# Performance work log

Measured on AMD Instinct MI355X. Metric: run time of the kernel, lower is better.

The kernel has to match this reference:

```python
import jax, jax.numpy as jnp
import numpy as np

B, N, F, U, S = 64, 4096, 2, 16, 2


def setup_inputs() -> dict:
    key = jax.random.key(0)
    ks = jax.random.split(key, 7)
    inputs = jax.random.normal(ks[0], (B, F * N), dtype=jnp.float32)
    state = jax.random.normal(ks[1], (B, U * N), dtype=jnp.float32)

    def random_walk(k):
        a = jax.random.uniform(k, (N, N), dtype=jnp.float32)
        return a / jnp.sum(a, axis=1, keepdims=True)  # row-stochastic like D^-1 A

    support0 = random_walk(ks[2])
    support1 = random_walk(ks[3])
    kshape = ((F + U) * S, U)
    scale = jnp.float32(1.0 / np.sqrt(kshape[0]))
    r_kernel = jax.random.normal(ks[4], kshape, dtype=jnp.float32) * scale
    u_kernel = jax.random.normal(ks[5], kshape, dtype=jnp.float32) * scale
    c_kernel = jax.random.normal(ks[6], kshape, dtype=jnp.float32) * scale
    return {"inputs": inputs, "state": state, "support0": support0,
            "support1": support1, "r_kernel": r_kernel, "u_kernel": u_kernel,
            "c_kernel": c_kernel}


def _diffuse(x, supports):
    # x: (B, C, N); K.dot(x, support.T)[b,c,m] = sum_n x[b,c,n] * support[m,n]
    return jnp.concatenate([jnp.einsum('bcn,mn->bcm', x, s) for s in supports], axis=1)


def reference(inputs, state, support0, support1, r_kernel, u_kernel, c_kernel):
    supports = (support0, support1)
    feats = inputs.reshape(B, F, N)
    prev = state.reshape(B, U, N)

    h = _diffuse(feats, supports).transpose(0, 2, 1)   # (B, N, S*F)
    st = _diffuse(prev, supports).transpose(0, 2, 1)   # (B, N, S*U)
    hs = jnp.concatenate([h, st], axis=-1)             # (B, N, S*(F+U))

    r = jax.nn.sigmoid(hs @ r_kernel)                  # (B, N, U)
    u = jax.nn.sigmoid(hs @ u_kernel)                  # (B, N, U)

    prev_t = prev.transpose(0, 2, 1)                   # (B, N, U)
    r_prev = (r * prev_t).transpose(0, 2, 1)           # (B, U, N)
    c_state = _diffuse(r_prev, supports).transpose(0, 2, 1)  # (B, N, S*U)
    c = jnp.tanh(jnp.concatenate([h, c_state], axis=-1) @ c_kernel)  # (B, N, U)

    z = u * prev_t + (1.0 - u) * c                     # (B, N, U)
    # original: activation=None -> linear, then K.reshape(output, (-1, units*num_nodes))
    return z.reshape(B, U * N)
```

## Files before the change

### kernel.cpp

```cpp
#include <hip/hip_runtime.h>
#include <cstdint>

#define KDIM 4096
#define NNODE 4096
#define TSTEPS 128

typedef __bf16 bf16x8 __attribute__((ext_vector_type(8)));
typedef float floatx4 __attribute__((ext_vector_type(4)));

__device__ __forceinline__ uint16_t f2b(float f) {
  union { float f; uint32_t u; } v; v.f = f;
  uint32_t u = v.u;
  return (uint16_t)((u + 0x7FFFu + ((u >> 16) & 1u)) >> 16);
}
__device__ __forceinline__ float b2f(uint16_t h) {
  union { uint32_t u; float f; } v; v.u = ((uint32_t)h) << 16; return v.f;
}
__device__ __forceinline__ uint32_t pack2(float a, float b) {
  return (uint32_t)f2b(a) | ((uint32_t)f2b(b) << 16);
}


__global__ __launch_bounds__(256) void cvt_supports(
    const float* __restrict__ s0, const float* __restrict__ s1,
    uint16_t* __restrict__ d0, uint16_t* __restrict__ d1) {
  const float* src = blockIdx.z ? s1 : s0;
  uint16_t* dst = blockIdx.z ? d1 : d0;
  const int c16 = blockIdx.x;
  const int t = blockIdx.y * 4 + (threadIdx.x >> 6);
  const int lane = threadIdx.x & 63;
  const int mr = lane & 15, q = lane >> 4;
  const float* p = src + (size_t)(c16 * 16 + mr) * KDIM + t * 32 + q * 8;
  float4 v0 = *(const float4*)p;
  float4 v1 = *(const float4*)(p + 4);
  uint4 o;
  o.x = pack2(v0.x, v0.y); o.y = pack2(v0.z, v0.w);
  o.z = pack2(v1.x, v1.y); o.w = pack2(v1.z, v1.w);
  *(uint4*)(dst + ((size_t)(c16 * 128 + t)) * 512 + (size_t)lane * 8) = o;
}

__global__ __launch_bounds__(256) void pack_x1(
    const float* __restrict__ inp, const float* __restrict__ st,
    uint16_t* __restrict__ X1) {
  const int r16 = blockIdx.x;
  const int t = blockIdx.y * 4 + (threadIdx.x >> 6);
  const int lane = threadIdx.x & 63;
  const int mr = lane & 15, q = lane >> 4;
  const int row = r16 * 16 + mr;
  int b = row / 18, c = row - b * 18;
  const float* p = (c < 2) ? (inp + (size_t)b * 8192 + (size_t)c * 4096)
                           : (st + (size_t)b * 65536 + (size_t)(c - 2) * 4096);
  p += t * 32 + q * 8;
  float4 v0 = *(const float4*)p;
  float4 v1 = *(const float4*)(p + 4);
  uint4 o;
  o.x = pack2(v0.x, v0.y); o.y = pack2(v0.z, v0.w);
  o.z = pack2(v1.x, v1.y); o.w = pack2(v1.z, v1.w);
  *(uint4*)(X1 + ((size_t)(r16 * 128 + t)) * 512 + (size_t)lane * 8) = o;
}

__device__ __forceinline__ void gl_lds16(const uint16_t* g, uint16_t* l) {
  __builtin_amdgcn_global_load_lds(
      (const __attribute__((address_space(1))) uint32_t*)g,
      (__attribute__((address_space(3))) uint32_t*)l, 16, 0, 0);
}

template <int MODE>
__global__ __launch_bounds__(512, 2) void gemm_frag(
    const uint16_t* __restrict__ Af, const uint16_t* __restrict__ S0f,
    const uint16_t* __restrict__ S1f, uint16_t* __restrict__ D) {
  constexpr int CPB   = (MODE == 1) ? 18 : 16;
  constexpr int OUTC  = (MODE == 1) ? 36 : 32;
  constexpr int MFR   = (MODE == 1) ? 9 : 8;
  constexpr int WM    = (MODE == 1) ? 1 : 2;
  constexpr int WN    = 8 / WM;
  constexpr int AR    = MFR / WM;
  constexpr int BR    = 16 / WN;
  constexpr int NREAL = MFR + 16;
  constexpr int SLOTS = (NREAL + 7) & ~7;
  constexpr int LPW   = SLOTS / 8;
  constexpr int NCH   = TSTEPS;

  __shared__ uint16_t sAB[4][SLOTS][512];

  const int lane = threadIdx.x & 63, wave = threadIdx.x >> 6;
  const int wr = wave / WN, wc = wave % WN;
  const int s = blockIdx.z;
  const uint16_t* __restrict__ Bf = s ? S1f : S0f;
  const int yF = blockIdx.y * MFR;
  const int xF = blockIdx.x * 16;

  const uint16_t* Gp[LPW];
#pragma unroll
  for (int i = 0; i < LPW; ++i) {
    int sid = wave * LPW + i;
    const uint16_t* base;
    int fr;
    if (sid < MFR)        { base = Af; fr = yF + sid; }
    else if (sid < NREAL) { base = Bf; fr = xF + sid - MFR; }
    else                  { base = Af; fr = yF; }
    Gp[i] = base + (size_t)fr * (TSTEPS * 512) + (size_t)lane * 8;
  }

  floatx4 acc[AR][BR];
#pragma unroll
  for (int i = 0; i < AR; ++i)
#pragma unroll
    for (int j = 0; j < BR; ++j) acc[i][j] = (floatx4){0.f, 0.f, 0.f, 0.f};

  auto STAGE = [&](int bi, int c) {
    uint16_t* l = &sAB[bi][wave * LPW][0];
    const size_t off = (size_t)c * 512;
#pragma unroll
    for (int i = 0; i < LPW; ++i)
      gl_lds16(Gp[i] + off, l + (size_t)i * 512);
  };

  auto LDREG = [&](int bi, bf16x8* a, bf16x8* b) {
    const uint16_t* base = &sAB[bi][0][lane * 8];
#pragma unroll
    for (int rt = 0; rt < AR; ++rt)
      a[rt] = *(const bf16x8*)(base + (size_t)(wr * AR + rt) * 512);
#pragma unroll
    for (int ct = 0; ct < BR; ++ct)
      b[ct] = *(const bf16x8*)(base + (size_t)(MFR + wc * BR + ct) * 512);
  };

  auto MFMAALL = [&](bf16x8* a, bf16x8* b) {
    __builtin_amdgcn_s_setprio(1);
#pragma unroll
    for (int rt = 0; rt < AR; ++rt)
#pragma unroll
      for (int ct = 0; ct < BR; ++ct)
        acc[rt][ct] = __builtin_amdgcn_mfma_f32_16x16x32_bf16(
            a[rt], b[ct], acc[rt][ct], 0, 0, 0);
    __builtin_amdgcn_s_setprio(0);
  };

  auto waitVM = [&] {
    if constexpr (MODE == 1) asm volatile("s_waitcnt vmcnt(8)" ::: "memory");
    else                     asm volatile("s_waitcnt vmcnt(6)" ::: "memory");
  };
  auto waitLG = [&] {
    if constexpr (MODE == 1) asm volatile("s_waitcnt lgkmcnt(11)" ::: "memory");
    else                     asm volatile("s_waitcnt lgkmcnt(8)" ::: "memory");
  };

  STAGE(0, 0);
  STAGE(1, 1);
  STAGE(2, 2);
  waitVM();
  __builtin_amdgcn_sched_barrier(0);
  __builtin_amdgcn_s_barrier();
  __builtin_amdgcn_sched_barrier(0);
  bf16x8 aA[AR], bA[BR], aB[AR], bB[BR];
  LDREG(0, aA, bA);

#define GITER(J, SB, RB, CA, CB, NA, NB)                                    \
  {                                                                         \
    int cl = c0 + 3 + (J);                                                  \
    if (cl > NCH - 1) cl = NCH - 1;       \
    STAGE((SB), cl);                                                        \
    waitVM();                                                               \
    __builtin_amdgcn_sched_barrier(0);                                      \
    __builtin_amdgcn_s_barrier();                                           \
    __builtin_amdgcn_sched_barrier(0);                                      \
    LDREG((RB), NA, NB);                                                    \
    waitLG();                                                               \
    __builtin_amdgcn_sched_barrier(0);                                      \
    MFMAALL(CA, CB);                                                        \
    __builtin_amdgcn_sched_barrier(0);                                      \
  }

  for (int m = 0; m < NCH / 4; ++m) {
    const int c0 = m * 4;
    GITER(0, 3, 1, aA, bA, aB, bB)
    GITER(1, 0, 2, aB, bB, aA, bA)
    GITER(2, 1, 3, aA, bA, aB, bB)
    GITER(3, 2, 0, aB, bB, aA, bA)
  }
#undef GITER

#pragma unroll
  for (int rt = 0; rt < AR; ++rt) {
#pragma unroll
    for (int r = 0; r < 4; ++r) {
      int rowg = (yF + wr * AR + rt) * 16 + (lane >> 4) * 4 + r;
      int b = rowg / CPB, c = rowg - b * CPB;
      int jj;
      if (MODE == 1) jj = (c < 2) ? (2 * s + c) : (4 + 16 * s + (c - 2));
      else jj = 16 * s + c;
      uint16_t* drow = D + (size_t)(b * OUTC + jj) * NNODE;
#pragma unroll
      for (int ct = 0; ct < BR; ++ct) {
        int colg = xF * 16 + (wc * BR + ct) * 16 + (lane & 15);
        drow[colg] = f2b(acc[rt][ct][r]);
      }
    }
  }
}

__global__ __launch_bounds__(256) void stage2(
    const uint16_t* __restrict__ P1, const float* __restrict__ state,
    const float* __restrict__ rk, const float* __restrict__ uk,
    uint16_t* __restrict__ X2f, float* __restrict__ U) {
  __shared__ float s_rk[576], s_uk[576];
  __shared__ uint16_t s_x2[16 * 264];
  for (int i = threadIdx.x; i < 576; i += 256) { s_rk[i] = rk[i]; s_uk[i] = uk[i]; }
  __syncthreads();
  const int b = blockIdx.x >> 4, nb = blockIdx.x & 15;
  const int i = threadIdx.x;
  const int n = nb * 256 + i;
  float hs[36];
  const uint16_t* p = P1 + (size_t)b * 36 * NNODE + n;
#pragma unroll
  for (int j = 0; j < 36; ++j)
    hs[j] = b2f(p[(size_t)j * NNODE]);
  float ar[16], au[16];
#pragma unroll
  for (int k = 0; k < 16; ++k) { ar[k] = 0.f; au[k] = 0.f; }
#pragma unroll
  for (int j = 0; j < 36; ++j) {
    float h = hs[j];
#pragma unroll
    for (int k = 0; k < 16; ++k) {
      ar[k] += h * s_rk[j * 16 + k];
      au[k] += h * s_uk[j * 16 + k];
    }
  }
  const float* sp = state + (size_t)b * 65536 + n;
#pragma unroll
  for (int k = 0; k < 16; ++k) {
    float r = 1.f / (1.f + __expf(-ar[k]));
    float uu = 1.f / (1.f + __expf(-au[k]));
    float prev = sp[(size_t)k * NNODE];
    s_x2[k * 264 + i] = f2b(r * prev);
    U[(size_t)(b * 16 + k) * NNODE + n] = uu;
  }
  __syncthreads();
  uint16_t* region = X2f + ((size_t)b * 128 + nb * 8) * 512;
#pragma unroll
  for (int rr = 0; rr < 2; ++rr) {
    int fid = rr * 256 + i;
    int kk = fid & 15, qq = (fid >> 4) & 3, tl = fid >> 6;
    uint4 v = *(const uint4*)&s_x2[kk * 264 + tl * 32 + qq * 8];
    *(uint4*)(region + (size_t)fid * 8) = v;
  }
}

__global__ __launch_bounds__(256) void stage4(
    const uint16_t* __restrict__ P1, const uint16_t* __restrict__ P3,
    const float* __restrict__ U, const float* __restrict__ state,
    const float* __restrict__ ck, float* __restrict__ out) {
  __shared__ float s_ck[576];
  for (int i = threadIdx.x; i < 576; i += 256) s_ck[i] = ck[i];
  __syncthreads();
  int idx = blockIdx.x * 256 + threadIdx.x;
  int b = idx >> 12, n = idx & 4095;
  float hv[36];
  const uint16_t* p1 = P1 + (size_t)b * 36 * NNODE + n;
#pragma unroll
  for (int j = 0; j < 4; ++j)
    hv[j] = b2f(p1[(size_t)j * NNODE]);
  const uint16_t* p3 = P3 + (size_t)b * 32 * NNODE + n;
#pragma unroll
  for (int j = 0; j < 32; ++j)
    hv[4 + j] = b2f(p3[(size_t)j * NNODE]);
  float ac[16];
#pragma unroll
  for (int k = 0; k < 16; ++k) ac[k] = 0.f;
#pragma unroll
  for (int j = 0; j < 36; ++j) {
    float h = hv[j];
#pragma unroll
    for (int k = 0; k < 16; ++k) ac[k] += h * s_ck[j * 16 + k];
  }
  const float* sp = state + (size_t)b * 65536 + n;
  const float* up = U + (size_t)b * 16 * NNODE + n;
  float z[16];
#pragma unroll
  for (int k = 0; k < 16; ++k) {
    float e = __expf(2.f * ac[k]);
    float c = 1.f - 2.f / (e + 1.f);
    float uu = up[(size_t)k * NNODE];
    float prev = sp[(size_t)k * NNODE];
    z[k] = uu * prev + (1.f - uu) * c;
  }
  float4* po = (float4*)(out + (size_t)b * 65536 + (size_t)n * 16);
#pragma unroll
  for (int k4 = 0; k4 < 4; ++k4)
    po[k4] = make_float4(z[k4 * 4], z[k4 * 4 + 1], z[k4 * 4 + 2], z[k4 * 4 + 3]);
}

extern "C" void kernel_launch(void* const* d_in, const int* in_sizes, int n_in,
                              void* d_out, int out_size, void* d_ws, size_t ws_size,
                              hipStream_t stream) {
  const float* inputs = (const float*)d_in[0];
  const float* state = (const float*)d_in[1];
  const float* s0 = (const float*)d_in[2];
  const float* s1 = (const float*)d_in[3];
  const float* rk = (const float*)d_in[4];
  const float* uk = (const float*)d_in[5];
  const float* ck = (const float*)d_in[6];
  float* out = (float*)d_out;
  char* ws = (char*)d_ws;

  uint16_t* S0f = (uint16_t*)(ws);
  uint16_t* S1f = (uint16_t*)(ws + 33554432);
  uint16_t* X1f = (uint16_t*)(ws + 67108864);
  uint16_t* X2f = (uint16_t*)(ws + 67108864);
  uint16_t* P1 = (uint16_t*)(ws + 76546048);
  float* U = (float*)(ws + 114294784);
  uint16_t* P3 = (uint16_t*)(ws + 131072000);

  cvt_supports<<<dim3(256, 32, 2), 256, 0, stream>>>(s0, s1, S0f, S1f);
  pack_x1<<<dim3(72, 32), 256, 0, stream>>>(inputs, state, X1f);
  gemm_frag<1><<<dim3(16, 8, 2), 512, 0, stream>>>(X1f, S0f, S1f, P1);
  stage2<<<1024, 256, 0, stream>>>(P1, state, rk, uk, X2f, U);
  gemm_frag<3><<<dim3(16, 8, 2), 512, 0, stream>>>(X2f, S0f, S1f, P3);
  stage4<<<1024, 256, 0, stream>>>(P1, P3, U, state, ck, out);
}
```

Baseline: 352.5 us.

## Split-K the second diffusion GEMM with larger M tiles and merge pack kernels

The second GEMM now doubles its per-block M fragment count (8 to 16) and splits the K dimension in two. Each half writes bf16 partials to separate buffers, and stage4 sums them. This gives more B reuse per block while keeping the grid at 256 blocks. The two fp32-to-bf16 pack kernels are also fused into one launch to cut launch overhead. In exchange, the extra partial buffer adds memory traffic, and rounding each partial to bf16 separately adds some precision loss.

```diff
diff --git a/kernel.cpp b/kernel.cpp
--- a/kernel.cpp
+++ b/kernel.cpp
@@ -21,42 +21,38 @@
 }
 
 
-__global__ __launch_bounds__(256) void cvt_supports(
+__global__ __launch_bounds__(256) void pack_all(
+    const float* __restrict__ inp, const float* __restrict__ st,
     const float* __restrict__ s0, const float* __restrict__ s1,
-    uint16_t* __restrict__ d0, uint16_t* __restrict__ d1) {
-  const float* src = blockIdx.z ? s1 : s0;
-  uint16_t* dst = blockIdx.z ? d1 : d0;
-  const int c16 = blockIdx.x;
+    uint16_t* __restrict__ X1, uint16_t* __restrict__ d0,
+    uint16_t* __restrict__ d1) {
   const int t = blockIdx.y * 4 + (threadIdx.x >> 6);
   const int lane = threadIdx.x & 63;
   const int mr = lane & 15, q = lane >> 4;
-  const float* p = src + (size_t)(c16 * 16 + mr) * KDIM + t * 32 + q * 8;
+  const float* p;
+  uint16_t* dst;
+  if (blockIdx.z < 2) {
+    const float* src = blockIdx.z ? s1 : s0;
+    uint16_t* d = blockIdx.z ? d1 : d0;
+    const int c16 = blockIdx.x;
+    p = src + (size_t)(c16 * 16 + mr) * KDIM + t * 32 + q * 8;
+    dst = d + ((size_t)(c16 * 128 + t)) * 512 + (size_t)lane * 8;
+  } else {
+    const int r16 = blockIdx.x;
+    if (r16 >= 72) return;
+    const int row = r16 * 16 + mr;
+    int b = row / 18, c = row - b * 18;
+    const float* pb = (c < 2) ? (inp + (size_t)b * 8192 + (size_t)c * 4096)
+                              : (st + (size_t)b * 65536 + (size_t)(c - 2) * 4096);
+    p = pb + t * 32 + q * 8;
+    dst = X1 + ((size_t)(r16 * 128 + t)) * 512 + (size_t)lane * 8;
+  }
   float4 v0 = *(const float4*)p;
   float4 v1 = *(const float4*)(p + 4);
   uint4 o;
   o.x = pack2(v0.x, v0.y); o.y = pack2(v0.z, v0.w);
   o.z = pack2(v1.x, v1.y); o.w = pack2(v1.z, v1.w);
-  *(uint4*)(dst + ((size_t)(c16 * 128 + t)) * 512 + (size_t)lane * 8) = o;
-}
-
-__global__ __launch_bounds__(256) void pack_x1(
-    const float* __restrict__ inp, const float* __restrict__ st,
-    uint16_t* __restrict__ X1) {
-  const int r16 = blockIdx.x;
-  const int t = blockIdx.y * 4 + (threadIdx.x >> 6);
-  const int lane = threadIdx.x & 63;
-  const int mr = lane & 15, q = lane >> 4;
-  const int row = r16 * 16 + mr;
-  int b = row / 18, c = row - b * 18;
-  const float* p = (c < 2) ? (inp + (size_t)b * 8192 + (size_t)c * 4096)
-                           : (st + (size_t)b * 65536 + (size_t)(c - 2) * 4096);
-  p += t * 32 + q * 8;
-  float4 v0 = *(const float4*)p;
-  float4 v1 = *(const float4*)(p + 4);
-  uint4 o;
-  o.x = pack2(v0.x, v0.y); o.y = pack2(v0.z, v0.w);
-  o.z = pack2(v1.x, v1.y); o.w = pack2(v1.z, v1.w);
-  *(uint4*)(X1 + ((size_t)(r16 * 128 + t)) * 512 + (size_t)lane * 8) = o;
+  *(uint4*)dst = o;
 }
 
 __device__ __forceinline__ void gl_lds16(const uint16_t* g, uint16_t* l) {
@@ -71,21 +67,26 @@
     const uint16_t* __restrict__ S1f, uint16_t* __restrict__ D) {
   constexpr int CPB   = (MODE == 1) ? 18 : 16;
   constexpr int OUTC  = (MODE == 1) ? 36 : 32;
-  constexpr int MFR   = (MODE == 1) ? 9 : 8;
+  constexpr int MFR   = (MODE == 1) ? 9 : 16;
   constexpr int WM    = (MODE == 1) ? 1 : 2;
   constexpr int WN    = 8 / WM;
   constexpr int AR    = MFR / WM;
   constexpr int BR    = 16 / WN;
   constexpr int NREAL = MFR + 16;
-  constexpr int SLOTS = (NREAL + 7) & ~7;
+  constexpr int SLOTS = 32;
   constexpr int LPW   = SLOTS / 8;
-  constexpr int NCH   = TSTEPS;
+  constexpr int KSP   = (MODE == 1) ? 1 : 2;
+  constexpr int NCH   = TSTEPS / KSP;
+  constexpr size_t PSTRIDE = (size_t)64 * OUTC * NNODE;
 
   __shared__ uint16_t sAB[4][SLOTS][512];
 
   const int lane = threadIdx.x & 63, wave = threadIdx.x >> 6;
   const int wr = wave / WN, wc = wave % WN;
-  const int s = blockIdx.z;
+  int s, ks;
+  if constexpr (MODE == 1) { s = blockIdx.z; ks = 0; }
+  else { s = blockIdx.z & 1; ks = blockIdx.z >> 1; }
+  const int tBeg = ks * NCH;
   const uint16_t* __restrict__ Bf = s ? S1f : S0f;
   const int yF = blockIdx.y * MFR;
   const int xF = blockIdx.x * 16;
@@ -99,7 +100,8 @@
     if (sid < MFR)        { base = Af; fr = yF + sid; }
     else if (sid < NREAL) { base = Bf; fr = xF + sid - MFR; }
     else                  { base = Af; fr = yF; }
-    Gp[i] = base + (size_t)fr * (TSTEPS * 512) + (size_t)lane * 8;
+    Gp[i] = base + (size_t)fr * (TSTEPS * 512) + (size_t)tBeg * 512 +
+            (size_t)lane * 8;
   }
 
   floatx4 acc[AR][BR];
@@ -138,12 +140,11 @@
   };
 
   auto waitVM = [&] {
-    if constexpr (MODE == 1) asm volatile("s_waitcnt vmcnt(8)" ::: "memory");
-    else                     asm volatile("s_waitcnt vmcnt(6)" ::: "memory");
+    asm volatile("s_waitcnt vmcnt(8)" ::: "memory");
   };
   auto waitLG = [&] {
     if constexpr (MODE == 1) asm volatile("s_waitcnt lgkmcnt(11)" ::: "memory");
-    else                     asm volatile("s_waitcnt lgkmcnt(8)" ::: "memory");
+    else                     asm volatile("s_waitcnt lgkmcnt(12)" ::: "memory");
   };
 
   STAGE(0, 0);
@@ -181,6 +182,8 @@
   }
 #undef GITER
 
+  uint16_t* Dp = D;
+  if constexpr (MODE == 3) Dp = D + (size_t)ks * PSTRIDE;
 #pragma unroll
   for (int rt = 0; rt < AR; ++rt) {
 #pragma unroll
@@ -190,7 +193,7 @@
       int jj;
       if (MODE == 1) jj = (c < 2) ? (2 * s + c) : (4 + 16 * s + (c - 2));
       else jj = 16 * s + c;
-      uint16_t* drow = D + (size_t)(b * OUTC + jj) * NNODE;
+      uint16_t* drow = Dp + (size_t)(b * OUTC + jj) * NNODE;
 #pragma unroll
       for (int ct = 0; ct < BR; ++ct) {
         int colg = xF * 16 + (wc * BR + ct) * 16 + (lane & 15);
@@ -252,6 +255,7 @@
     const uint16_t* __restrict__ P1, const uint16_t* __restrict__ P3,
     const float* __restrict__ U, const float* __restrict__ state,
     const float* __restrict__ ck, float* __restrict__ out) {
+  constexpr size_t PS3 = (size_t)64 * 32 * NNODE;
   __shared__ float s_ck[576];
   for (int i = threadIdx.x; i < 576; i += 256) s_ck[i] = ck[i];
   __syncthreads();
@@ -265,7 +269,7 @@
   const uint16_t* p3 = P3 + (size_t)b * 32 * NNODE + n;
 #pragma unroll
   for (int j = 0; j < 32; ++j)
-    hv[4 + j] = b2f(p3[(size_t)j * NNODE]);
+    hv[4 + j] = b2f(p3[(size_t)j * NNODE]) + b2f(p3[PS3 + (size_t)j * NNODE]);
   float ac[16];
 #pragma unroll
   for (int k = 0; k < 16; ++k) ac[k] = 0.f;
@@ -313,10 +317,10 @@
   float* U = (float*)(ws + 114294784);
   uint16_t* P3 = (uint16_t*)(ws + 131072000);
 
-  cvt_supports<<<dim3(256, 32, 2), 256, 0, stream>>>(s0, s1, S0f, S1f);
-  pack_x1<<<dim3(72, 32), 256, 0, stream>>>(inputs, state, X1f);
+  pack_all<<<dim3(256, 32, 3), 256, 0, stream>>>(inputs, state, s0, s1,
+                                                 X1f, S0f, S1f);
   gemm_frag<1><<<dim3(16, 8, 2), 512, 0, stream>>>(X1f, S0f, S1f, P1);
   stage2<<<1024, 256, 0, stream>>>(P1, state, rk, uk, X2f, U);
-  gemm_frag<3><<<dim3(16, 8, 2), 512, 0, stream>>>(X2f, S0f, S1f, P3);
+  gemm_frag<3><<<dim3(16, 4, 4), 512, 0, stream>>>(X2f, S0f, S1f, P3);
   stage4<<<1024, 256, 0, stream>>>(P1, P3, U, state, ck, out);
 }
```

New measurement: 342.4 us. 2.9% less time.
